# Kernel tuning notes

Measured on AMD Instinct MI355X. Metric: run time of the kernel, lower is better.

## Reference

```python
import jax, jax.numpy as jnp
import numpy as np

N_NODES = 100000
N_EDGES = 1600000
IN_DIM = 128
HID = 64
NUM_GRAPHS = 2048
NUM_CLASSES = 1


def setup_inputs() -> dict:
    key = jax.random.key(0)
    ks = jax.random.split(key, 16)
    x = jax.random.normal(ks[0], (N_NODES, IN_DIM), dtype=jnp.float32)
    edge_index = jax.random.randint(ks[1], (2, N_EDGES), 0, N_NODES, dtype=jnp.int64)
    batch_index = jnp.sort(jax.random.randint(ks[2], (N_NODES,), 0, NUM_GRAPHS, dtype=jnp.int64))
    # GCNConv weights (glorot-ish scale)
    def lin(k, fi, fo):
        return jax.random.normal(k, (fi, fo), dtype=jnp.float32) / np.sqrt(fi)
    W1 = lin(ks[3], IN_DIM, HID); b1 = jnp.zeros((HID,), jnp.float32)
    W2 = lin(ks[4], HID, HID);    b2 = jnp.zeros((HID,), jnp.float32)
    W3 = lin(ks[5], HID, HID);    b3 = jnp.zeros((HID,), jnp.float32)
    W4 = lin(ks[6], HID, HID);    b4 = jnp.zeros((HID,), jnp.float32)
    Wout = lin(ks[7], 2 * HID, NUM_CLASSES); bout = jnp.zeros((NUM_CLASSES,), jnp.float32)
    return {"x": x, "edge_index": edge_index, "batch_index": batch_index,
            "W1": W1, "b1": b1, "W2": W2, "b2": b2, "W3": W3, "b3": b3,
            "W4": W4, "b4": b4, "Wout": Wout, "bout": bout}


def _gcn_conv(x, W, b, src, dst, norm, n):
    # PyG GCNConv: linear transform, then D^-1/2 (A+I) D^-1/2 aggregation, then bias
    h = x @ W                                   # [N, F_out]
    msg = h[src] * norm[:, None]                # [E+N, F_out] gather + scale
    agg = jax.ops.segment_sum(msg, dst, num_segments=n)
    return agg + b


def reference(x, edge_index, batch_index, W1, b1, W2, b2, W3, b3, W4, b4, Wout, bout):
    n = x.shape[0]
    loops = jnp.arange(n, dtype=edge_index.dtype)
    src = jnp.concatenate([edge_index[0], loops])  # add self-loops
    dst = jnp.concatenate([edge_index[1], loops])
    deg = jax.ops.segment_sum(jnp.ones_like(dst, dtype=x.dtype), dst, num_segments=n)
    dis = jax.lax.rsqrt(deg)                       # deg >= 1 due to self-loops
    norm = dis[src] * dis[dst]

    h = x
    for (W, b) in ((W1, b1), (W2, b2), (W3, b3), (W4, b4)):
        h = jax.nn.relu(_gcn_conv(h, W, b, src, dst, norm, n))

    # global mean pool + global max pool per graph
    counts = jax.ops.segment_sum(jnp.ones((n,), h.dtype), batch_index, num_segments=NUM_GRAPHS)
    mean = jax.ops.segment_sum(h, batch_index, num_segments=NUM_GRAPHS) / jnp.maximum(counts, 1.0)[:, None]
    mx = jax.ops.segment_max(h, batch_index, num_segments=NUM_GRAPHS)
    mx = jnp.where(counts[:, None] > 0, mx, 0.0)
    pooled = jnp.concatenate([mean, mx], axis=1)   # [G, 2*HID]

    out = pooled @ Wout + bout                     # [G, 1]
    return (out, pooled)
```

## Files before the change

kernel.cpp:

```cpp
#include <hip/hip_runtime.h>
#include <hip/hip_fp16.h>

#define N_NODES 100000
#define IN_DIM 128
#define HID 64
#define NUM_GRAPHS 2048
#define CNE_MAX (1600000 + 7 * N_NODES)
#define BROWS 128
#define NBUCK ((N_NODES + BROWS - 1) / BROWS)
#define NCHUNK 256
#define TOTP (NBUCK * NCHUNK)
#define CAP 4096

typedef _Float16 h8 __attribute__((ext_vector_type(8)));
typedef float f4 __attribute__((ext_vector_type(4)));

#define SLICE_E ((size_t)(N_NODES + 1) * 16)

__device__ __forceinline__ float2 u2f2(unsigned u) {
    __half2 h = *reinterpret_cast<__half2*>(&u);
    return __half22float2(h);
}


__global__ __launch_bounds__(256) void hist_partial(const int* __restrict__ dst,
                                                    int* __restrict__ partial,
                                                    int E, int chunk,
                                                    unsigned* __restrict__ tmppad) {
    __shared__ int lh[NBUCK];
    int t = threadIdx.x, c = blockIdx.x;
    if (c == 0 && t < 32)
        tmppad[(size_t)(t >> 3) * ((N_NODES + 1) * 8) + (size_t)N_NODES * 8 + (t & 7)] = 0;
    for (int b = t; b < NBUCK; b += 256) lh[b] = 0;
    __syncthreads();
    int lo = c * chunk, hi = min(lo + chunk, E);
    for (int i = lo + t; i < hi; i += 256) atomicAdd(&lh[dst[i] >> 7], 1);
    __syncthreads();
    for (int b = t; b < NBUCK; b += 256) partial[b * NCHUNK + c] = lh[b];
}

__global__ void scan1(const int* __restrict__ counts, int* __restrict__ out1,
                      int* __restrict__ bsum, int n, int pad8) {
    __shared__ int s[256];
    int t = threadIdx.x;
    int base = blockIdx.x * 1024 + t * 4;
    int v[4];
#pragma unroll
    for (int i = 0; i < 4; i++) {
        int c = (base + i < n) ? counts[base + i] : 0;
        v[i] = pad8 ? ((c + 7) & ~7) : c;
    }
    int tsum = v[0] + v[1] + v[2] + v[3];
    s[t] = tsum;
    __syncthreads();
    for (int off = 1; off < 256; off <<= 1) {
        int tv = (t >= off) ? s[t - off] : 0;
        __syncthreads();
        s[t] += tv;
        __syncthreads();
    }
    int excl = s[t] - tsum;
    if (t == 255) bsum[blockIdx.x] = s[255];
    int run = excl;
#pragma unroll
    for (int i = 0; i < 4; i++) {
        run += v[i];
        if (base + i < n) out1[base + i] = run;
    }
}

__device__ __forceinline__ void inline_bscan(const int* __restrict__ bsum, int nb, int* s) {
    int t = threadIdx.x;
    int v = (t < nb) ? bsum[t] : 0;
    s[t] = v;
    __syncthreads();
    for (int off = 1; off < 256; off <<= 1) {
        int tv = (t >= off) ? s[t - off] : 0;
        __syncthreads();
        s[t] += tv;
        __syncthreads();
    }
    int excl = s[t] - v;
    __syncthreads();
    s[t] = excl;
    __syncthreads();
}

__global__ __launch_bounds__(256) void scan3(int* __restrict__ row_ptr,
                                             const int* __restrict__ bsum, int nb, int n) {
    __shared__ int s[256];
    inline_bscan(bsum, nb, s);
    int i = blockIdx.x * blockDim.x + threadIdx.x;
    if (i == 0) row_ptr[0] = 0;
    if (i < n) row_ptr[i + 1] += s[i >> 10];
}

__global__ __launch_bounds__(256) void scan3p(const int* __restrict__ partial,
                                              const int* __restrict__ pincl,
                                              const int* __restrict__ bsum, int nb,
                                              int* __restrict__ base,
                                              int* __restrict__ part_off, int E) {
    __shared__ int s[256];
    inline_bscan(bsum, nb, s);
    int i = blockIdx.x * blockDim.x + threadIdx.x;
    if (i < TOTP) {
        int v = pincl[i] + s[i >> 10] - partial[i];
        base[i] = v;
        if ((i & (NCHUNK - 1)) == 0) part_off[i / NCHUNK] = v;
    }
    if (i == 0) part_off[NBUCK] = E;
}

__global__ __launch_bounds__(256) void partition_edges(const int* __restrict__ src,
                                                       const int* __restrict__ dst,
                                                       const int* __restrict__ base,
                                                       unsigned* __restrict__ part,
                                                       int E, int chunk) {
    __shared__ int cur[NBUCK];
    int t = threadIdx.x, c = blockIdx.x;
    for (int b = t; b < NBUCK; b += 256) cur[b] = base[b * NCHUNK + c];
    __syncthreads();
    int lo = c * chunk, hi = min(lo + chunk, E);
    for (int i = lo + t; i < hi; i += 256) {
        int s = src[i], d = dst[i];
        int pos = atomicAdd(&cur[d >> 7], 1);
        part[pos] = (unsigned)s | ((unsigned)(d & (BROWS - 1)) << 17);
    }
}

__global__ __launch_bounds__(256) void deg_dis(const unsigned* __restrict__ part,
                                               const int* __restrict__ part_off,
                                               int* __restrict__ pdeg,
                                               float* __restrict__ dis, int n) {
    __shared__ int cnt[BROWS];
    int t = threadIdx.x, b = blockIdx.x;
    int r0 = b * BROWS;
    if (t < BROWS) cnt[t] = 0;
    __syncthreads();
    for (int i = part_off[b] + t; i < part_off[b + 1]; i += 256)
        atomicAdd(&cnt[part[i] >> 17], 1);
    __syncthreads();
    int nrows = min(BROWS, n - r0);
    if (t < nrows) {
        int dg = cnt[t];
        pdeg[r0 + t] = dg;
        dis[r0 + t] = rsqrtf((float)(dg + 1));
    }
}

__global__ __launch_bounds__(256) void build_csr(const unsigned* __restrict__ part,
                                                 const int* __restrict__ part_off,
                                                 const int* __restrict__ row_ptr,
                                                 unsigned* __restrict__ cne, int n) {
    __shared__ int fill[BROWS];
    __shared__ unsigned stage[CAP];
    int b = blockIdx.x;
    int r0 = b * BROWS;
    int t = threadIdx.x;
    int nrows = min(BROWS, n - r0);
    int base = row_ptr[r0];
    int region = row_ptr[r0 + nrows] - base;
    for (int r = t; r < nrows; r += 256) fill[r] = row_ptr[r0 + r] - base;
    int i0 = part_off[b], i1 = part_off[b + 1];
    if (region <= CAP) {
        for (int i = t; i < region; i += 256) stage[i] = (unsigned)N_NODES << 5;
        __syncthreads();
        for (int i = i0 + t; i < i1; i += 256) {
            unsigned pe = part[i];
            int pos = atomicAdd(&fill[pe >> 17], 1);
            stage[pos] = (pe & 0x1FFFFu) << 5;
        }
        __syncthreads();
        for (int i = t; i < region; i += 256) cne[base + i] = stage[i];
    } else {
        for (int i = t; i < region; i += 256) cne[base + i] = (unsigned)N_NODES << 5;
        __syncthreads();
        for (int i = i0 + t; i < i1; i += 256) {
            unsigned pe = part[i];
            int pos = atomicAdd(&fill[pe >> 17], 1);
            cne[base + pos] = (pe & 0x1FFFFu) << 5;
        }
    }
}


template <int K, typename XT, bool SIN>
__global__ __launch_bounds__(256) void gemm_mfma(const XT* __restrict__ X,
                                                 const float* __restrict__ W,
                                                 const float* __restrict__ dis,
                                                 __half* __restrict__ out, int n) {
    const int KS = K / 32;
    int wave = threadIdx.x >> 6, lane = threadIdx.x & 63;
    int quad = lane >> 4, l16 = lane & 15;
    h8 b[4][KS];
#pragma unroll
    for (int ct = 0; ct < 4; ct++)
#pragma unroll
        for (int ks = 0; ks < KS; ks++)
#pragma unroll
            for (int j = 0; j < 8; j++)
                b[ct][ks][j] = (_Float16)W[(ks * 32 + quad * 8 + j) * HID + ct * 16 + l16];
    int ntile = n >> 4;
    int wpb = blockDim.x >> 6;
    int stride = gridDim.x * wpb;
    for (int rt = blockIdx.x * wpb + wave; rt < ntile; rt += stride) {
        int row0 = rt << 4;
        f4 acc[4];
#pragma unroll
        for (int ct = 0; ct < 4; ct++) acc[ct] = (f4)(0.f);
#pragma unroll
        for (int ks = 0; ks < KS; ks++) {
            h8 a;
            if constexpr (SIN) {
                a = *(const h8*)(X + (size_t)(ks * 2 + (quad >> 1)) * SLICE_E +
                                 (size_t)(row0 + l16) * 16 + (quad & 1) * 8);
            } else {
                const XT* xr = X + (size_t)(row0 + l16) * K + quad * 8 + ks * 32;
                float4 xa = *(const float4*)(xr);
                float4 xb = *(const float4*)(xr + 4);
                a[0] = (_Float16)xa.x; a[1] = (_Float16)xa.y;
                a[2] = (_Float16)xa.z; a[3] = (_Float16)xa.w;
                a[4] = (_Float16)xb.x; a[5] = (_Float16)xb.y;
                a[6] = (_Float16)xb.z; a[7] = (_Float16)xb.w;
            }
#pragma unroll
            for (int ct = 0; ct < 4; ct++)
                acc[ct] = __builtin_amdgcn_mfma_f32_16x16x32_f16(a, b[ct][ks], acc[ct], 0, 0, 0);
        }
        int r0 = row0 + quad * 4;
        float4 dv = *(const float4*)(dis + r0);
        float dd[4] = {dv.x, dv.y, dv.z, dv.w};
#pragma unroll
        for (int reg = 0; reg < 4; reg++) {
#pragma unroll
            for (int ct = 0; ct < 4; ct++)
                out[(size_t)ct * SLICE_E + (size_t)(r0 + reg) * 16 + l16] =
                    __float2half(dd[reg] * acc[ct][reg]);
        }
    }
}

template <typename OutT>
__global__ __launch_bounds__(256) void aggregate_slice(const __half* __restrict__ tmp,
                                                       const float* __restrict__ dis,
                                                       const int* __restrict__ row_ptr,
                                                       const unsigned* __restrict__ cne,
                                                       const float* __restrict__ bias,
                                                       OutT* __restrict__ out, int n) {
    int wave = threadIdx.x >> 6, lane = threadIdx.x & 63;
    int m = lane & 7, rq = lane >> 3;
    int slice = blockIdx.x & 3;
    const char* tb = (const char*)(tmp + (size_t)slice * SLICE_E);
    int c = 8 * (m & 1) + 4 * ((m >> 1) & 1) + 2 * ((m >> 2) & 1);
    float2 blv = *(const float2*)(bias + slice * 16 + c);
    int sblk = blockIdx.x >> 2;
    int nspb = gridDim.x >> 2;
    int ntasks = (n + 7) >> 3;
    for (int task = sblk * 4 + wave; task < ntasks; task += nspb * 4) {
        int row = task * 8 + rq;
        float a[16];
#pragma unroll
        for (int i = 0; i < 16; i++) a[i] = 0.f;
        int sE = row_ptr[row];
        int ng = (row_ptr[row + 1] - sE) >> 3;
        const unsigned* ci = cne + sE + m;
        unsigned off = (ng > 0) ? ci[0] : 0u;
        for (int g = 0; g < ng; g++) {
            uint4 q0 = *(const uint4*)(tb + off);
            uint4 q1 = *(const uint4*)(tb + off + 16);
            if (g + 1 < ng) off = ci[(g + 1) * 8];
            float2 f;
            f = u2f2(q0.x); a[0] += f.x;  a[1] += f.y;
            f = u2f2(q0.y); a[2] += f.x;  a[3] += f.y;
            f = u2f2(q0.z); a[4] += f.x;  a[5] += f.y;
            f = u2f2(q0.w); a[6] += f.x;  a[7] += f.y;
            f = u2f2(q1.x); a[8] += f.x;  a[9] += f.y;
            f = u2f2(q1.y); a[10] += f.x; a[11] += f.y;
            f = u2f2(q1.z); a[12] += f.x; a[13] += f.y;
            f = u2f2(q1.w); a[14] += f.x; a[15] += f.y;
        }
        float v8[8], v4[4], v2[2];
#pragma unroll
        for (int i = 0; i < 8; i++) {
            float keep = (m & 1) ? a[i + 8] : a[i];
            float send = (m & 1) ? a[i] : a[i + 8];
            v8[i] = keep + __shfl_xor(send, 1);
        }
#pragma unroll
        for (int i = 0; i < 4; i++) {
            float keep = (m & 2) ? v8[i + 4] : v8[i];
            float send = (m & 2) ? v8[i] : v8[i + 4];
            v4[i] = keep + __shfl_xor(send, 2);
        }
#pragma unroll
        for (int i = 0; i < 2; i++) {
            float keep = (m & 4) ? v4[i + 2] : v4[i];
            float send = (m & 4) ? v4[i] : v4[i + 2];
            v2[i] = keep + __shfl_xor(send, 4);
        }
        float dr = dis[row];
        float2 sf = u2f2(*(const unsigned*)(tb + (size_t)row * 32 + 2 * c));
        float vx = fmaxf(dr * (sf.x + v2[0]) + blv.x, 0.f);
        float vy = fmaxf(dr * (sf.y + v2[1]) + blv.y, 0.f);
        if constexpr (__is_same(OutT, __half)) {
            *(__half2*)(out + (size_t)slice * SLICE_E + (size_t)row * 16 + c) =
                __floats2half2_rn(vx, vy);
        } else {
            *(float2*)(out + (size_t)slice * SLICE_E + (size_t)row * 16 + c) =
                make_float2(vx, vy);
        }
    }
}

__global__ __launch_bounds__(256) void pool_kernel(const float* __restrict__ h,
                                                   const int* __restrict__ batch,
                                                   const float* __restrict__ Wout,
                                                   const float* __restrict__ bout,
                                                   float* __restrict__ d_out, int n) {
    __shared__ float ssum[4][64];
    __shared__ float smax[4][64];
    int g = blockIdx.x;
    int wave = threadIdx.x >> 6, j = threadIdx.x & 63;
    size_t cbase = (size_t)(j >> 4) * SLICE_E + (j & 15);
    int lo = 0, hi = n;
    while (lo < hi) { int mid = (lo + hi) >> 1; if (batch[mid] < g) lo = mid + 1; else hi = mid; }
    int start = lo;
    hi = n;
    while (lo < hi) { int mid = (lo + hi) >> 1; if (batch[mid] < g + 1) lo = mid + 1; else hi = mid; }
    int end = lo;

    float sum = 0.f, mx = 0.f;
    for (int i = start + wave; i < end; i += 4) {
        float v = h[cbase + (size_t)i * 16];
        sum += v;
        mx = fmaxf(mx, v);
    }
    ssum[wave][j] = sum;
    smax[wave][j] = mx;
    __syncthreads();
    if (wave == 0) {
        sum = (ssum[0][j] + ssum[1][j]) + (ssum[2][j] + ssum[3][j]);
        mx = fmaxf(fmaxf(smax[0][j], smax[1][j]), fmaxf(smax[2][j], smax[3][j]));
        float cnt = (float)(end - start);
        float mean = sum / fmaxf(cnt, 1.f);
        float* pooled = d_out + NUM_GRAPHS;
        pooled[(size_t)g * (2 * HID) + j] = mean;
        pooled[(size_t)g * (2 * HID) + HID + j] = mx;
        float c = mean * Wout[j] + mx * Wout[HID + j];
#pragma unroll
        for (int off = 32; off; off >>= 1) c += __shfl_down(c, off);
        if (j == 0) d_out[g] = c + bout[0];
    }
}


extern "C" void kernel_launch(void* const* d_in, const int* in_sizes, int n_in,
                              void* d_out, int out_size, void* d_ws, size_t ws_size,
                              hipStream_t stream) {
    const float* x    = (const float*)d_in[0];
    const int*   edge = (const int*)d_in[1];
    const int*   batch= (const int*)d_in[2];
    const float* W1 = (const float*)d_in[3];  const float* b1 = (const float*)d_in[4];
    const float* W2 = (const float*)d_in[5];  const float* b2 = (const float*)d_in[6];
    const float* W3 = (const float*)d_in[7];  const float* b3 = (const float*)d_in[8];
    const float* W4 = (const float*)d_in[9];  const float* b4 = (const float*)d_in[10];
    const float* Wout = (const float*)d_in[11]; const float* bout = (const float*)d_in[12];
    float* out = (float*)d_out;

    const int N = N_NODES;
    const int E = in_sizes[1] / 2;
    const int* src = edge;
    const int* dst = edge + E;
    const int chunk = (E + NCHUNK - 1) / NCHUNK;

    char* p = (char*)d_ws;
    auto alloc = [&](size_t bytes) -> char* {
        char* r = p;
        p += (bytes + 255) & ~(size_t)255;
        return r;
    };
    int*      pdeg     = (int*)alloc((size_t)N * 4);
    int*      row_ptr  = (int*)alloc((size_t)(N + 1) * 4);
    int*      partial  = (int*)alloc((size_t)TOTP * 4);
    int*      pincl    = (int*)alloc((size_t)TOTP * 4);
    int*      pbase    = (int*)alloc((size_t)TOTP * 4);
    int*      part_off = (int*)alloc((size_t)(NBUCK + 1) * 4);
    unsigned* part     = (unsigned*)alloc((size_t)1600000 * 4);
    unsigned* cne      = (unsigned*)alloc((size_t)CNE_MAX * 4);
    float*    dis      = (float*)alloc((size_t)N * 4);
    int*      bsum     = (int*)alloc(256 * 4);
    __half*   tmp      = (__half*)alloc(SLICE_E * 4 * 2);
    float*    hA       = (float*)alloc(SLICE_E * 4 * 4);
    __half*   hH       = (__half*)hA;

    hist_partial<<<NCHUNK, 256, 0, stream>>>(dst, partial, E, chunk, (unsigned*)tmp);
    int nbp = (TOTP + 1023) / 1024;
    scan1<<<nbp, 256, 0, stream>>>(partial, pincl, bsum, TOTP, 0);
    scan3p<<<(TOTP + 255) / 256, 256, 0, stream>>>(partial, pincl, bsum, nbp, pbase, part_off, E);
    partition_edges<<<NCHUNK, 256, 0, stream>>>(src, dst, pbase, part, E, chunk);
    deg_dis<<<NBUCK, 256, 0, stream>>>(part, part_off, pdeg, dis, N);

    int nb = (N + 1023) / 1024;
    scan1<<<nb, 256, 0, stream>>>(pdeg, row_ptr + 1, bsum, N, 1);
    scan3<<<(N + 255) / 256, 256, 0, stream>>>(row_ptr, bsum, nb, N);
    build_csr<<<NBUCK, 256, 0, stream>>>(part, part_off, row_ptr, cne, N);

    const int AGG_BLOCKS = 2048;
    const int GEMM_BLOCKS = 1024;

    gemm_mfma<IN_DIM, float, false><<<GEMM_BLOCKS, 256, 0, stream>>>(x, W1, dis, tmp, N);
    aggregate_slice<__half><<<AGG_BLOCKS, 256, 0, stream>>>(tmp, dis, row_ptr, cne, b1, hH, N);
    gemm_mfma<HID, _Float16, true><<<GEMM_BLOCKS, 256, 0, stream>>>((_Float16*)hH, W2, dis, tmp, N);
    aggregate_slice<__half><<<AGG_BLOCKS, 256, 0, stream>>>(tmp, dis, row_ptr, cne, b2, hH, N);
    gemm_mfma<HID, _Float16, true><<<GEMM_BLOCKS, 256, 0, stream>>>((_Float16*)hH, W3, dis, tmp, N);
    aggregate_slice<__half><<<AGG_BLOCKS, 256, 0, stream>>>(tmp, dis, row_ptr, cne, b3, hH, N);
    gemm_mfma<HID, _Float16, true><<<GEMM_BLOCKS, 256, 0, stream>>>((_Float16*)hH, W4, dis, tmp, N);
    aggregate_slice<float><<<AGG_BLOCKS, 256, 0, stream>>>(tmp, dis, row_ptr, cne, b4, hA, N);

    pool_kernel<<<NUM_GRAPHS, 256, 0, stream>>>(hA, batch, Wout, bout, out, N);
}
```

Baseline: 410.3 us.

## Remap aggregation lanes to 4 per row with register-pipelined 8-edge gathers

The aggregate kernel now assigns 4 lanes per row, each handling 4 feature columns, instead of 8 lanes per row splitting edges. Each lane reads all 8 edge offsets of a group with two uint4 loads and gathers 8-byte chunks. The next group's gathers are issued before the current group is accumulated, giving software prefetch, and the cross-lane shuffle reduction is removed. The trade-off is narrower per-lane gathers (8 B instead of 32 B) and more registers, and it relies on the padded sentinel offset Z for empty rows and on n being a multiple of 16.

```diff
diff --git a/kernel.cpp b/kernel.cpp
--- a/kernel.cpp
+++ b/kernel.cpp
@@ -248,66 +248,81 @@
                                                        const float* __restrict__ bias,
                                                        OutT* __restrict__ out, int n) {
     int wave = threadIdx.x >> 6, lane = threadIdx.x & 63;
-    int m = lane & 7, rq = lane >> 3;
+    int m2 = lane & 3, rq = lane >> 2;
     int slice = blockIdx.x & 3;
-    const char* tb = (const char*)(tmp + (size_t)slice * SLICE_E);
-    int c = 8 * (m & 1) + 4 * ((m >> 1) & 1) + 2 * ((m >> 2) & 1);
-    float2 blv = *(const float2*)(bias + slice * 16 + c);
+    const char* tb = (const char*)(tmp + (size_t)slice * SLICE_E) + 8 * m2;
+    float4 blv = *(const float4*)(bias + slice * 16 + 4 * m2);
     int sblk = blockIdx.x >> 2;
     int nspb = gridDim.x >> 2;
-    int ntasks = (n + 7) >> 3;
-    for (int task = sblk * 4 + wave; task < ntasks; task += nspb * 4) {
-        int row = task * 8 + rq;
-        float a[16];
-#pragma unroll
-        for (int i = 0; i < 16; i++) a[i] = 0.f;
-        int sE = row_ptr[row];
-        int ng = (row_ptr[row + 1] - sE) >> 3;
-        const unsigned* ci = cne + sE + m;
-        unsigned off = (ng > 0) ? ci[0] : 0u;
-        for (int g = 0; g < ng; g++) {
-            uint4 q0 = *(const uint4*)(tb + off);
-            uint4 q1 = *(const uint4*)(tb + off + 16);
-            if (g + 1 < ng) off = ci[(g + 1) * 8];
+    int ntask = n >> 4;
+    const unsigned Z = (unsigned)N_NODES << 5;
+    for (int task = sblk * 4 + wave; task < ntask; task += nspb * 4) {
+        int row = (task << 4) + rq;
+        float dr = dis[row];
+        int sE = row_ptr[row], eE = row_ptr[row + 1];
+        int ng = (eE - sE) >> 3;
+        const uint4* ip = (const uint4*)(cne + sE);
+        uint4 A0, A1;
+        if (ng > 0) { A0 = ip[0]; A1 = ip[1]; }
+        else { A0 = make_uint4(Z, Z, Z, Z); A1 = make_uint4(Z, Z, Z, Z); }
+        uint2 g0 = *(const uint2*)(tb + A0.x);
+        uint2 g1 = *(const uint2*)(tb + A0.y);
+        uint2 g2 = *(const uint2*)(tb + A0.z);
+        uint2 g3 = *(const uint2*)(tb + A0.w);
+        uint2 g4 = *(const uint2*)(tb + A1.x);
+        uint2 g5 = *(const uint2*)(tb + A1.y);
+        uint2 g6 = *(const uint2*)(tb + A1.z);
+        uint2 g7 = *(const uint2*)(tb + A1.w);
+        float a0 = 0.f, a1 = 0.f, a2 = 0.f, a3 = 0.f;
+        uint4 B0, B1;
+        if (ng > 1) { B0 = ip[2]; B1 = ip[3]; }
+        for (int g = 1; g < ng; g++) {
+            uint2 u0 = *(const uint2*)(tb + B0.x);
+            uint2 u1 = *(const uint2*)(tb + B0.y);
+            uint2 u2 = *(const uint2*)(tb + B0.z);
+            uint2 u3 = *(const uint2*)(tb + B0.w);
+            uint2 u4 = *(const uint2*)(tb + B1.x);
+            uint2 u5 = *(const uint2*)(tb + B1.y);
+            uint2 u6 = *(const uint2*)(tb + B1.z);
+            uint2 u7 = *(const uint2*)(tb + B1.w);
+            if (g + 1 < ng) { B0 = ip[2 * g + 2]; B1 = ip[2 * g + 3]; }
             float2 f;
-            f = u2f2(q0.x); a[0] += f.x;  a[1] += f.y;
-            f = u2f2(q0.y); a[2] += f.x;  a[3] += f.y;
-            f = u2f2(q0.z); a[4] += f.x;  a[5] += f.y;
-            f = u2f2(q0.w); a[6] += f.x;  a[7] += f.y;
-            f = u2f2(q1.x); a[8] += f.x;  a[9] += f.y;
-            f = u2f2(q1.y); a[10] += f.x; a[11] += f.y;
-            f = u2f2(q1.z); a[12] += f.x; a[13] += f.y;
-            f = u2f2(q1.w); a[14] += f.x; a[15] += f.y;
-        }
-        float v8[8], v4[4], v2[2];
-#pragma unroll
-        for (int i = 0; i < 8; i++) {
-            float keep = (m & 1) ? a[i + 8] : a[i];
-            float send = (m & 1) ? a[i] : a[i + 8];
-            v8[i] = keep + __shfl_xor(send, 1);
-        }
-#pragma unroll
-        for (int i = 0; i < 4; i++) {
-            float keep = (m & 2) ? v8[i + 4] : v8[i];
-            float send = (m & 2) ? v8[i] : v8[i + 4];
-            v4[i] = keep + __shfl_xor(send, 2);
-        }
-#pragma unroll
-        for (int i = 0; i < 2; i++) {
-            float keep = (m & 4) ? v4[i + 2] : v4[i];
-            float send = (m & 4) ? v4[i] : v4[i + 2];
-            v2[i] = keep + __shfl_xor(send, 4);
-        }
-        float dr = dis[row];
-        float2 sf = u2f2(*(const unsigned*)(tb + (size_t)row * 32 + 2 * c));
-        float vx = fmaxf(dr * (sf.x + v2[0]) + blv.x, 0.f);
-        float vy = fmaxf(dr * (sf.y + v2[1]) + blv.y, 0.f);
+            f = u2f2(g0.x); a0 += f.x; a1 += f.y; f = u2f2(g0.y); a2 += f.x; a3 += f.y;
+            f = u2f2(g1.x); a0 += f.x; a1 += f.y; f = u2f2(g1.y); a2 += f.x; a3 += f.y;
+            f = u2f2(g2.x); a0 += f.x; a1 += f.y; f = u2f2(g2.y); a2 += f.x; a3 += f.y;
+            f = u2f2(g3.x); a0 += f.x; a1 += f.y; f = u2f2(g3.y); a2 += f.x; a3 += f.y;
+            f = u2f2(g4.x); a0 += f.x; a1 += f.y; f = u2f2(g4.y); a2 += f.x; a3 += f.y;
+            f = u2f2(g5.x); a0 += f.x; a1 += f.y; f = u2f2(g5.y); a2 += f.x; a3 += f.y;
+            f = u2f2(g6.x); a0 += f.x; a1 += f.y; f = u2f2(g6.y); a2 += f.x; a3 += f.y;
+            f = u2f2(g7.x); a0 += f.x; a1 += f.y; f = u2f2(g7.y); a2 += f.x; a3 += f.y;
+            g0 = u0; g1 = u1; g2 = u2; g3 = u3;
+            g4 = u4; g5 = u5; g6 = u6; g7 = u7;
+        }
+        {
+            float2 f;
+            f = u2f2(g0.x); a0 += f.x; a1 += f.y; f = u2f2(g0.y); a2 += f.x; a3 += f.y;
+            f = u2f2(g1.x); a0 += f.x; a1 += f.y; f = u2f2(g1.y); a2 += f.x; a3 += f.y;
+            f = u2f2(g2.x); a0 += f.x; a1 += f.y; f = u2f2(g2.y); a2 += f.x; a3 += f.y;
+            f = u2f2(g3.x); a0 += f.x; a1 += f.y; f = u2f2(g3.y); a2 += f.x; a3 += f.y;
+            f = u2f2(g4.x); a0 += f.x; a1 += f.y; f = u2f2(g4.y); a2 += f.x; a3 += f.y;
+            f = u2f2(g5.x); a0 += f.x; a1 += f.y; f = u2f2(g5.y); a2 += f.x; a3 += f.y;
+            f = u2f2(g6.x); a0 += f.x; a1 += f.y; f = u2f2(g6.y); a2 += f.x; a3 += f.y;
+            f = u2f2(g7.x); a0 += f.x; a1 += f.y; f = u2f2(g7.y); a2 += f.x; a3 += f.y;
+        }
+        uint2 sv = *(const uint2*)(tb + (size_t)row * 32);
+        float2 s01 = u2f2(sv.x), s23 = u2f2(sv.y);
+        float v0 = fmaxf(dr * (s01.x + a0) + blv.x, 0.f);
+        float v1 = fmaxf(dr * (s01.y + a1) + blv.y, 0.f);
+        float v2 = fmaxf(dr * (s23.x + a2) + blv.z, 0.f);
+        float v3 = fmaxf(dr * (s23.y + a3) + blv.w, 0.f);
         if constexpr (__is_same(OutT, __half)) {
-            *(__half2*)(out + (size_t)slice * SLICE_E + (size_t)row * 16 + c) =
-                __floats2half2_rn(vx, vy);
+            __half2 p01 = __floats2half2_rn(v0, v1);
+            __half2 p23 = __floats2half2_rn(v2, v3);
+            *(uint2*)(out + (size_t)slice * SLICE_E + (size_t)row * 16 + 4 * m2) =
+                make_uint2(*(unsigned*)&p01, *(unsigned*)&p23);
         } else {
-            *(float2*)(out + (size_t)slice * SLICE_E + (size_t)row * 16 + c) =
-                make_float2(vx, vy);
+            *(float4*)(out + (size_t)slice * SLICE_E + (size_t)row * 16 + 4 * m2) =
+                make_float4(v0, v1, v2, v3);
         }
     }
 }
```

New measurement: 402.2 us. -2.0%, faster.
